# Optimization experiments

Hardware: AMD Instinct MI355X
Metric: run time of the kernel (lower is better)

The kernel has to match this reference:

```python
import jax, jax.numpy as jnp
import numpy as np

SIZES = [384, 160, 128, 96, 1]   # aev_length followed by hidden sizes (ANI-1 config)
N_SPECIES = 4                    # H, C, N, O
N_LAYERS = 4
CELU_ALPHA = 0.1
B, A = 128, 512                  # molecules, atoms per molecule


def setup_inputs() -> dict:
    key = jax.random.key(0)
    ks = jax.random.split(key, 2 + 2 * N_LAYERS)
    inp = {
        "fullaev": jax.random.normal(ks[0], (B, A, SIZES[0]), dtype=jnp.float32),
        "species": jax.random.randint(ks[1], (A,), 0, N_SPECIES, dtype=jnp.int32),
    }
    # Per-species stacked Linear params, torch default init: U(-1/sqrt(fan_in), 1/sqrt(fan_in))
    for l in range(N_LAYERS):
        bound = 1.0 / np.sqrt(SIZES[l])
        inp[f"W{l}"] = jax.random.uniform(ks[2 + 2 * l], (N_SPECIES, SIZES[l + 1], SIZES[l]),
                                          dtype=jnp.float32, minval=-bound, maxval=bound)
        inp[f"b{l}"] = jax.random.uniform(ks[3 + 2 * l], (N_SPECIES, SIZES[l + 1]),
                                          dtype=jnp.float32, minval=-bound, maxval=bound)
    return inp


def reference(fullaev, species, W0, b0, W1, b1, W2, b2, W3, b3):
    # fullaev: [B, A, aev_len]; species: [A] int route ids.
    # Equivalent to the per-atom Python loop: each atom goes through its
    # species' MLP; gather the per-atom weight matrices and do one batched GEMM per layer.
    Ws = (W0, W1, W2, W3)
    bs = (b0, b1, b2, b3)
    y = fullaev
    for l in range(N_LAYERS):
        Wa = Ws[l][species]          # [A, out, in] gathered per atom
        ba = bs[l][species]          # [A, out]
        y = jnp.einsum('bai,aoi->bao', y, Wa) + ba[None, :, :]
        if l < N_LAYERS - 1:
            y = jax.nn.celu(y, alpha=CELU_ALPHA)
    # stack over atoms + sum reducer over atom dim, then squeeze -> [B]
    return jnp.squeeze(jnp.sum(y, axis=1), axis=-1)
```

## Files before the change

kernel.cpp:

```cpp
#include <hip/hip_runtime.h>
#include <hip/hip_bf16.h>


typedef float f32x4 __attribute__((ext_vector_type(4)));
typedef short s16x8 __attribute__((ext_vector_type(8)));

#define NMOL   128
#define NATOM  512
#define AEV    384
#define MT     64
#define Y0LD   168
#define Y1LD   136
#define Y2LD   104
#define Y1_OFF 10752
#define RED_OFF 19456

#define PL0    61440
#define PL1    20480
#define PL2    12288
#define BASE0  0
#define BASE1  245760
#define BASE2  327680
#define WP_BYTE_OFF 262144

typedef const __attribute__((address_space(1))) void* gas_ptr;
typedef __attribute__((address_space(3))) void* las_ptr;

__device__ __forceinline__ ushort f2bf(float f) {
    uint u = __float_as_uint(f);
    return (ushort)((u + 0x7fffu + ((u >> 16) & 1u)) >> 16);
}
__device__ __forceinline__ float bf2f(ushort h) {
    return __uint_as_float(((uint)h) << 16);
}
__device__ __forceinline__ float celu_f(float v) {
    return fmaxf(v, 0.0f) + fminf(0.1f * (__expf(10.0f * v) - 1.0f), 0.0f);
}
__device__ __forceinline__ uint pk2bf(float x, float y) {
    __hip_bfloat162 h2;
    h2.x = __float2bfloat16(x);
    h2.y = __float2bfloat16(y);
    return *(uint*)&h2;
}

__global__ __launch_bounds__(256) void prep_kernel(
    const float* __restrict__ W0, const float* __restrict__ W1,
    const float* __restrict__ W2, ushort* __restrict__ Wp)
{
    const int idx = blockIdx.x * 256 + threadIdx.x;
    int n, k0, KS;
    size_t base;
    const float* src;
    if (idx < 30720) {
        const int s = idx / 7680, r = idx % 7680;
        n = r / 48; k0 = (r % 48) * 8; KS = 12;
        src = W0 + (size_t)idx * 8;
        base = BASE0 + (size_t)s * PL0;
    } else if (idx < 40960) {
        const int i2 = idx - 30720;
        const int s = i2 / 2560, r = i2 % 2560;
        n = r / 20; k0 = (r % 20) * 8; KS = 5;
        src = W1 + (size_t)i2 * 8;
        base = BASE1 + (size_t)s * PL1;
    } else {
        const int i2 = idx - 40960;
        const int s = i2 / 1536, r = i2 % 1536;
        n = r / 16; k0 = (r % 16) * 8; KS = 4;
        src = W2 + (size_t)i2 * 8;
        base = BASE2 + (size_t)s * PL2;
    }
    const float4 v0 = *(const float4*)(src);
    const float4 v1 = *(const float4*)(src + 4);
    const size_t fo = (size_t)((((n >> 4) * KS + (k0 >> 5)) * 64
                                + ((k0 & 31) >> 3) * 16 + (n & 15)) * 8);
    uint4 w;
    w.x = pk2bf(v0.x, v0.y);
    w.y = pk2bf(v0.z, v0.w);
    w.z = pk2bf(v1.x, v1.y);
    w.w = pk2bf(v1.z, v1.w);
    *(uint4*)(Wp + base + fo) = w;
}

__global__ __attribute__((amdgpu_flat_work_group_size(512, 512),
                          amdgpu_waves_per_eu(8, 8)))
void ani_mfma_kernel(
    const float* __restrict__ aev, const int* __restrict__ species,
    const ushort* __restrict__ Wp,
    const float* __restrict__ b0, const float* __restrict__ b1,
    const float* __restrict__ b2,
    const float* __restrict__ W3, const float* __restrict__ b3,
    float* __restrict__ partial)
{
    __shared__ __align__(16) ushort smem[20480];

    const int bid  = blockIdx.x;
    const int a    = bid >> 1;
    const int half = bid & 1;
    const int tid  = threadIdx.x;
    const int lane = tid & 63;
    const int wid  = tid >> 6;
    const int mgrp = wid >> 2;
    const int ngrp = wid & 3;
    const bool has3 = (ngrp < 2);

    const int s = species[a];
    const ushort* Bh0 = Wp + BASE0 + (size_t)s * PL0;
    const ushort* Bh1 = Wp + BASE1 + (size_t)s * PL1;
    const ushort* Bh2 = Wp + BASE2 + (size_t)s * PL2;
    const float* b0s = b0 + s * 160;
    const float* b1s = b1 + s * 128;
    const float* b2s = b2 + s * 96;
    const float* w3s = W3 + s * 96;
    const float  bb3 = b3[s];

    ushort* y0buf = smem;
    ushort* y1buf = smem + Y1_OFF;
    ushort* y2buf = smem;

    const int mol8 = lane >> 3;
    const int swz  = (lane & 7) ^ mol8;
    const char* gsrc = (const char*)(aev
        + ((size_t)(half * MT + wid * 8 + mol8) * NATOM + a) * AEV) + swz * 16;
    const int ldsbase = wid * 2048;

    const f32x4 zero = {0.f, 0.f, 0.f, 0.f};
    f32x4 acc[2][3];
    #pragma unroll
    for (int mf = 0; mf < 2; ++mf)
        #pragma unroll
        for (int ti = 0; ti < 3; ++ti) acc[mf][ti] = zero;

    {
        const int r0 = mgrp * 32 + (lane & 15);
        const int c2 = (lane >> 4) * 2;

        __builtin_amdgcn_global_load_lds((gas_ptr)(gsrc),
            (las_ptr)((char*)smem + ldsbase), 16, 0, 0);
        __builtin_amdgcn_global_load_lds((gas_ptr)(gsrc + 128),
            (las_ptr)((char*)smem + ldsbase + 1024), 16, 0, 0);
        __syncthreads();

        #pragma unroll
        for (int t = 0; t < 6; ++t) {
            if (t < 5) {
                const char* g = gsrc + (t + 1) * 256;
                char* d = (char*)smem + ((t + 1) & 1) * 16384 + ldsbase;
                __builtin_amdgcn_global_load_lds((gas_ptr)(g),       (las_ptr)(d),        16, 0, 0);
                __builtin_amdgcn_global_load_lds((gas_ptr)(g + 128), (las_ptr)(d + 1024), 16, 0, 0);
            }
            const float* Xb = (const float*)((const char*)smem + (t & 1) * 16384);
            #pragma unroll
            for (int gs = 0; gs < 2; ++gs) {
                const int gks = t * 2 + gs;
                const s16x8 bh0 = *(const s16x8*)(
                    Bh0 + ((size_t)((ngrp    ) * 12 + gks) * 64 + lane) * 8);
                const s16x8 bh1 = *(const s16x8*)(
                    Bh0 + ((size_t)((ngrp + 4) * 12 + gks) * 64 + lane) * 8);
                s16x8 bh2;
                if (has3) bh2 = *(const s16x8*)(
                    Bh0 + ((size_t)((ngrp + 8) * 12 + gks) * 64 + lane) * 8);

                s16x8 ah[2];
                #pragma unroll
                for (int mf = 0; mf < 2; ++mf) {
                    const int r = r0 + mf * 16;
                    const float* rp = Xb + (r >> 3) * 512 + gs * 256 + (r & 7) * 32;
                    const f32x4 v0 = *(const f32x4*)(rp + (((c2    ) ^ (r & 7)) * 4));
                    const f32x4 v1 = *(const f32x4*)(rp + (((c2 + 1) ^ (r & 7)) * 4));
                    union { s16x8 v; uint u[4]; } rr;
                    rr.u[0] = pk2bf(v0.x, v0.y);
                    rr.u[1] = pk2bf(v0.z, v0.w);
                    rr.u[2] = pk2bf(v1.x, v1.y);
                    rr.u[3] = pk2bf(v1.z, v1.w);
                    ah[mf] = rr.v;
                }
                acc[0][0] = __builtin_amdgcn_mfma_f32_16x16x32_bf16(ah[0], bh0, acc[0][0], 0, 0, 0);
                acc[1][0] = __builtin_amdgcn_mfma_f32_16x16x32_bf16(ah[1], bh0, acc[1][0], 0, 0, 0);
                acc[0][1] = __builtin_amdgcn_mfma_f32_16x16x32_bf16(ah[0], bh1, acc[0][1], 0, 0, 0);
                acc[1][1] = __builtin_amdgcn_mfma_f32_16x16x32_bf16(ah[1], bh1, acc[1][1], 0, 0, 0);
                if (has3) {
                    acc[0][2] = __builtin_amdgcn_mfma_f32_16x16x32_bf16(ah[0], bh2, acc[0][2], 0, 0, 0);
                    acc[1][2] = __builtin_amdgcn_mfma_f32_16x16x32_bf16(ah[1], bh2, acc[1][2], 0, 0, 0);
                }
            }
            __syncthreads();
        }
    }

    #pragma unroll
    for (int ti = 0; ti < 3; ++ti) {
        if (ti < 2 || has3) {
            const int n = (ngrp + 4 * ti) * 16 + (lane & 15);
            const float bv = b0s[n];
            #pragma unroll
            for (int mf = 0; mf < 2; ++mf) {
                #pragma unroll
                for (int r = 0; r < 4; ++r) {
                    const int row = mgrp * 32 + mf * 16 + (lane >> 4) * 4 + r;
                    y0buf[row * Y0LD + n] = f2bf(celu_f(acc[mf][ti][r] + bv));
                }
            }
        }
    }
    __syncthreads();

    f32x4 acc1[2][2];
    #pragma unroll
    for (int mf = 0; mf < 2; ++mf) { acc1[mf][0] = zero; acc1[mf][1] = zero; }
    {
        const ushort* arow0 = y0buf + (mgrp * 32 + (lane & 15)) * Y0LD + (lane >> 4) * 8;
        #pragma unroll
        for (int ks = 0; ks < 5; ++ks) {
            s16x8 ah[2];
            ah[0] = *(const s16x8*)(arow0 + ks * 32);
            ah[1] = *(const s16x8*)(arow0 + 16 * Y0LD + ks * 32);
            const s16x8 bh0 = *(const s16x8*)(
                Bh1 + ((size_t)((ngrp    ) * 5 + ks) * 64 + lane) * 8);
            const s16x8 bh1 = *(const s16x8*)(
                Bh1 + ((size_t)((ngrp + 4) * 5 + ks) * 64 + lane) * 8);
            acc1[0][0] = __builtin_amdgcn_mfma_f32_16x16x32_bf16(ah[0], bh0, acc1[0][0], 0, 0, 0);
            acc1[1][0] = __builtin_amdgcn_mfma_f32_16x16x32_bf16(ah[1], bh0, acc1[1][0], 0, 0, 0);
            acc1[0][1] = __builtin_amdgcn_mfma_f32_16x16x32_bf16(ah[0], bh1, acc1[0][1], 0, 0, 0);
            acc1[1][1] = __builtin_amdgcn_mfma_f32_16x16x32_bf16(ah[1], bh1, acc1[1][1], 0, 0, 0);
        }
    }

    #pragma unroll
    for (int t = 0; t < 2; ++t) {
        const int n = (ngrp + 4 * t) * 16 + (lane & 15);
        const float bv = b1s[n];
        #pragma unroll
        for (int mf = 0; mf < 2; ++mf) {
            #pragma unroll
            for (int r = 0; r < 4; ++r) {
                const int row = mgrp * 32 + mf * 16 + (lane >> 4) * 4 + r;
                y1buf[row * Y1LD + n] = f2bf(celu_f(acc1[mf][t][r] + bv));
            }
        }
    }
    __syncthreads();

    f32x4 acc2[2][2];
    #pragma unroll
    for (int mf = 0; mf < 2; ++mf) { acc2[mf][0] = zero; acc2[mf][1] = zero; }
    {
        const ushort* arow0 = y1buf + (mgrp * 32 + (lane & 15)) * Y1LD + (lane >> 4) * 8;
        #pragma unroll
        for (int ks = 0; ks < 4; ++ks) {
            s16x8 ah[2];
            ah[0] = *(const s16x8*)(arow0 + ks * 32);
            ah[1] = *(const s16x8*)(arow0 + 16 * Y1LD + ks * 32);
            const s16x8 bh0 = *(const s16x8*)(
                Bh2 + ((size_t)((ngrp) * 4 + ks) * 64 + lane) * 8);
            acc2[0][0] = __builtin_amdgcn_mfma_f32_16x16x32_bf16(ah[0], bh0, acc2[0][0], 0, 0, 0);
            acc2[1][0] = __builtin_amdgcn_mfma_f32_16x16x32_bf16(ah[1], bh0, acc2[1][0], 0, 0, 0);
            if (has3) {
                const s16x8 bh1 = *(const s16x8*)(
                    Bh2 + ((size_t)((ngrp + 4) * 4 + ks) * 64 + lane) * 8);
                acc2[0][1] = __builtin_amdgcn_mfma_f32_16x16x32_bf16(ah[0], bh1, acc2[0][1], 0, 0, 0);
                acc2[1][1] = __builtin_amdgcn_mfma_f32_16x16x32_bf16(ah[1], bh1, acc2[1][1], 0, 0, 0);
            }
        }
    }

    #pragma unroll
    for (int t = 0; t < 2; ++t) {
        if (t == 0 || has3) {
            const int n = (ngrp + 4 * t) * 16 + (lane & 15);
            const float bv = b2s[n];
            #pragma unroll
            for (int mf = 0; mf < 2; ++mf) {
                #pragma unroll
                for (int r = 0; r < 4; ++r) {
                    const int row = mgrp * 32 + mf * 16 + (lane >> 4) * 4 + r;
                    y2buf[row * Y2LD + n] = f2bf(celu_f(acc2[mf][t][r] + bv));
                }
            }
        }
    }
    __syncthreads();

    {
        float* red = (float*)(smem + RED_OFF);
        const int m = tid & (MT - 1);
        const int q = tid >> 6;
        float accv = 0.f;
        #pragma unroll
        for (int ii = 0; ii < 12; ++ii) {
            const int i = q * 12 + ii;
            accv = fmaf(w3s[i], bf2f(y2buf[m * Y2LD + i]), accv);
        }
        red[q * MT + m] = accv;
        __syncthreads();
        if (tid < MT) {
            float sm = bb3;
            #pragma unroll
            for (int qq = 0; qq < 8; ++qq) sm += red[qq * MT + tid];
            partial[(size_t)a * NMOL + half * MT + tid] = sm;
        }
    }
}

__global__ __launch_bounds__(256) void reduce_kernel(
    const float* __restrict__ partial, float* __restrict__ out)
{
    __shared__ float red[256];
    const int m = blockIdx.x;
    const int t = threadIdx.x;
    float sv = partial[(size_t)t * NMOL + m] + partial[(size_t)(t + 256) * NMOL + m];
    red[t] = sv;
    __syncthreads();
    #pragma unroll
    for (int w = 128; w > 0; w >>= 1) {
        if (t < w) red[t] += red[t + w];
        __syncthreads();
    }
    if (t == 0) out[m] = red[0];
}

extern "C" void kernel_launch(void* const* d_in, const int* in_sizes, int n_in,
                              void* d_out, int out_size, void* d_ws, size_t ws_size,
                              hipStream_t stream) {
    const float* aev     = (const float*)d_in[0];
    const int*   species = (const int*)  d_in[1];
    const float* W0 = (const float*)d_in[2];
    const float* b0 = (const float*)d_in[3];
    const float* W1 = (const float*)d_in[4];
    const float* b1 = (const float*)d_in[5];
    const float* W2 = (const float*)d_in[6];
    const float* b2 = (const float*)d_in[7];
    const float* W3 = (const float*)d_in[8];
    const float* b3 = (const float*)d_in[9];
    float* out     = (float*)d_out;
    float* partial = (float*)d_ws;
    ushort* Wp     = (ushort*)((char*)d_ws + WP_BYTE_OFF);

    prep_kernel<<<184, 256, 0, stream>>>(W0, W1, W2, Wp);
    ani_mfma_kernel<<<NATOM * 2, 512, 0, stream>>>(aev, species, Wp,
                                                   b0, b1, b2, W3, b3, partial);
    reduce_kernel<<<NMOL, 256, 0, stream>>>(partial, out);
}
```

Baseline: 44.12 us.

## Stage per-species weight fragments into LDS via async global-to-LDS loads

The bf16 weight fragments for all three MFMA layers are now copied into LDS with global_load_lds. Layer 0 is double-buffered alongside the AEV tiles, and layers 1 and 2 are staged while the previous epilogue runs. Before, every wave read the weights directly from global memory. The layer-0 packing in the prep kernel is reordered so each k-step slab is contiguous. LDS use grows from about 40KB to 72KB, the waves-per-EU target drops from 8 to 4, and the shared buffers get a new layout. The aim is to take weight-load latency off the MFMA path, at the cost of lower occupancy and an extra barrier.

```diff
diff --git a/kernel.cpp b/kernel.cpp
--- a/kernel.cpp
+++ b/kernel.cpp
@@ -12,8 +12,6 @@
 #define Y0LD   168
 #define Y1LD   136
 #define Y2LD   104
-#define Y1_OFF 10752
-#define RED_OFF 19456
 
 #define PL0    61440
 #define PL1    20480
@@ -48,31 +46,35 @@
     const float* __restrict__ W2, ushort* __restrict__ Wp)
 {
     const int idx = blockIdx.x * 256 + threadIdx.x;
-    int n, k0, KS;
-    size_t base;
+    size_t fo, base;
     const float* src;
     if (idx < 30720) {
         const int s = idx / 7680, r = idx % 7680;
-        n = r / 48; k0 = (r % 48) * 8; KS = 12;
+        const int n = r / 48, k0 = (r % 48) * 8;
+        const int t = k0 >> 6, h = (k0 >> 5) & 1;
+        fo = (size_t)t * 10240 + ((n >> 4) * 2 + h) * 512
+           + (((k0 & 31) >> 3) * 16 + (n & 15)) * 8;
         src = W0 + (size_t)idx * 8;
         base = BASE0 + (size_t)s * PL0;
     } else if (idx < 40960) {
         const int i2 = idx - 30720;
         const int s = i2 / 2560, r = i2 % 2560;
-        n = r / 20; k0 = (r % 20) * 8; KS = 5;
+        const int n = r / 20, k0 = (r % 20) * 8;
+        fo = (size_t)(((n >> 4) * 5 + (k0 >> 5)) * 64
+           + ((k0 & 31) >> 3) * 16 + (n & 15)) * 8;
         src = W1 + (size_t)i2 * 8;
         base = BASE1 + (size_t)s * PL1;
     } else {
         const int i2 = idx - 40960;
         const int s = i2 / 1536, r = i2 % 1536;
-        n = r / 16; k0 = (r % 16) * 8; KS = 4;
+        const int n = r / 16, k0 = (r % 16) * 8;
+        fo = (size_t)(((n >> 4) * 4 + (k0 >> 5)) * 64
+           + ((k0 & 31) >> 3) * 16 + (n & 15)) * 8;
         src = W2 + (size_t)i2 * 8;
         base = BASE2 + (size_t)s * PL2;
     }
     const float4 v0 = *(const float4*)(src);
     const float4 v1 = *(const float4*)(src + 4);
-    const size_t fo = (size_t)((((n >> 4) * KS + (k0 >> 5)) * 64
-                                + ((k0 & 31) >> 3) * 16 + (n & 15)) * 8);
     uint4 w;
     w.x = pk2bf(v0.x, v0.y);
     w.y = pk2bf(v0.z, v0.w);
@@ -82,7 +84,7 @@
 }
 
 __global__ __attribute__((amdgpu_flat_work_group_size(512, 512),
-                          amdgpu_waves_per_eu(8, 8)))
+                          amdgpu_waves_per_eu(4, 4)))
 void ani_mfma_kernel(
     const float* __restrict__ aev, const int* __restrict__ species,
     const ushort* __restrict__ Wp,
@@ -91,7 +93,8 @@
     const float* __restrict__ W3, const float* __restrict__ b3,
     float* __restrict__ partial)
 {
-    __shared__ __align__(16) ushort smem[20480];
+    __shared__ __align__(16) char smem8[73728];
+    ushort* smem_u = (ushort*)smem8;
 
     const int bid  = blockIdx.x;
     const int a    = bid >> 1;
@@ -113,9 +116,10 @@
     const float* w3s = W3 + s * 96;
     const float  bb3 = b3[s];
 
-    ushort* y0buf = smem;
-    ushort* y1buf = smem + Y1_OFF;
-    ushort* y2buf = smem;
+    ushort* y0buf = smem_u;
+    ushort* y1buf = smem_u;
+    ushort* y2buf = smem_u + 8704;
+    const ushort* BL = smem_u + 16384;
 
     const int mol8 = lane >> 3;
     const int swz  = (lane & 7) ^ mol8;
@@ -123,6 +127,19 @@
         + ((size_t)(half * MT + wid * 8 + mol8) * NATOM + a) * AEV) + swz * 16;
     const int ldsbase = wid * 2048;
 
+    auto stage_a = [&](int t, int b) {
+        const char* g = gsrc + t * 256;
+        char* d = smem8 + b * 16384 + ldsbase;
+        __builtin_amdgcn_global_load_lds((gas_ptr)(g),       (las_ptr)(d),        16, 0, 0);
+        __builtin_amdgcn_global_load_lds((gas_ptr)(g + 128), (las_ptr)(d + 1024), 16, 0, 0);
+    };
+    auto stage_b = [&](const ushort* gbase, int nchunks, int ldsbyte) {
+        for (int c = wid; c < nchunks; c += 8)
+            __builtin_amdgcn_global_load_lds(
+                (gas_ptr)((const char*)gbase + c * 1024 + lane * 16),
+                (las_ptr)(smem8 + ldsbyte + c * 1024), 16, 0, 0);
+    };
+
     const f32x4 zero = {0.f, 0.f, 0.f, 0.f};
     f32x4 acc[2][3];
     #pragma unroll
@@ -134,31 +151,25 @@
         const int r0 = mgrp * 32 + (lane & 15);
         const int c2 = (lane >> 4) * 2;
 
-        __builtin_amdgcn_global_load_lds((gas_ptr)(gsrc),
-            (las_ptr)((char*)smem + ldsbase), 16, 0, 0);
-        __builtin_amdgcn_global_load_lds((gas_ptr)(gsrc + 128),
-            (las_ptr)((char*)smem + ldsbase + 1024), 16, 0, 0);
+        stage_a(0, 0);
+        stage_b(Bh0, 20, 32768);
         __syncthreads();
 
         #pragma unroll
-        for (int t = 0; t < 6; ++t) {
-            if (t < 5) {
-                const char* g = gsrc + (t + 1) * 256;
-                char* d = (char*)smem + ((t + 1) & 1) * 16384 + ldsbase;
-                __builtin_amdgcn_global_load_lds((gas_ptr)(g),       (las_ptr)(d),        16, 0, 0);
-                __builtin_amdgcn_global_load_lds((gas_ptr)(g + 128), (las_ptr)(d + 1024), 16, 0, 0);
-            }
-            const float* Xb = (const float*)((const char*)smem + (t & 1) * 16384);
+        for (int tt = 0; tt < 6; ++tt) {
+            if (tt < 5) {
+                stage_a(tt + 1, (tt + 1) & 1);
+                stage_b(Bh0 + (size_t)(tt + 1) * 10240, 20,
+                        32768 + ((tt + 1) & 1) * 20480);
+            }
+            const float*  Xb = (const float*)(smem8 + (tt & 1) * 16384);
+            const ushort* Bl = BL + (tt & 1) * 10240;
             #pragma unroll
             for (int gs = 0; gs < 2; ++gs) {
-                const int gks = t * 2 + gs;
-                const s16x8 bh0 = *(const s16x8*)(
-                    Bh0 + ((size_t)((ngrp    ) * 12 + gks) * 64 + lane) * 8);
-                const s16x8 bh1 = *(const s16x8*)(
-                    Bh0 + ((size_t)((ngrp + 4) * 12 + gks) * 64 + lane) * 8);
+                const s16x8 bh0 = *(const s16x8*)(Bl + ((ngrp      * 2 + gs) * 512) + lane * 8);
+                const s16x8 bh1 = *(const s16x8*)(Bl + (((ngrp + 4) * 2 + gs) * 512) + lane * 8);
                 s16x8 bh2;
-                if (has3) bh2 = *(const s16x8*)(
-                    Bh0 + ((size_t)((ngrp + 8) * 12 + gks) * 64 + lane) * 8);
+                if (has3) bh2 = *(const s16x8*)(Bl + (((ngrp + 8) * 2 + gs) * 512) + lane * 8);
 
                 s16x8 ah[2];
                 #pragma unroll
@@ -187,6 +198,7 @@
         }
     }
 
+    stage_b(Bh1, 40, 32768);
     #pragma unroll
     for (int ti = 0; ti < 3; ++ti) {
         if (ti < 2 || has3) {
@@ -214,17 +226,17 @@
             s16x8 ah[2];
             ah[0] = *(const s16x8*)(arow0 + ks * 32);
             ah[1] = *(const s16x8*)(arow0 + 16 * Y0LD + ks * 32);
-            const s16x8 bh0 = *(const s16x8*)(
-                Bh1 + ((size_t)((ngrp    ) * 5 + ks) * 64 + lane) * 8);
-            const s16x8 bh1 = *(const s16x8*)(
-                Bh1 + ((size_t)((ngrp + 4) * 5 + ks) * 64 + lane) * 8);
+            const s16x8 bh0 = *(const s16x8*)(BL + ((ngrp      * 5 + ks) * 512) + lane * 8);
+            const s16x8 bh1 = *(const s16x8*)(BL + (((ngrp + 4) * 5 + ks) * 512) + lane * 8);
             acc1[0][0] = __builtin_amdgcn_mfma_f32_16x16x32_bf16(ah[0], bh0, acc1[0][0], 0, 0, 0);
             acc1[1][0] = __builtin_amdgcn_mfma_f32_16x16x32_bf16(ah[1], bh0, acc1[1][0], 0, 0, 0);
             acc1[0][1] = __builtin_amdgcn_mfma_f32_16x16x32_bf16(ah[0], bh1, acc1[0][1], 0, 0, 0);
             acc1[1][1] = __builtin_amdgcn_mfma_f32_16x16x32_bf16(ah[1], bh1, acc1[1][1], 0, 0, 0);
         }
     }
-
+    __syncthreads();
+
+    stage_b(Bh2, 24, 32768);
     #pragma unroll
     for (int t = 0; t < 2; ++t) {
         const int n = (ngrp + 4 * t) * 16 + (lane & 15);
@@ -250,13 +262,11 @@
             s16x8 ah[2];
             ah[0] = *(const s16x8*)(arow0 + ks * 32);
             ah[1] = *(const s16x8*)(arow0 + 16 * Y1LD + ks * 32);
-            const s16x8 bh0 = *(const s16x8*)(
-                Bh2 + ((size_t)((ngrp) * 4 + ks) * 64 + lane) * 8);
+            const s16x8 bh0 = *(const s16x8*)(BL + ((ngrp * 4 + ks) * 512) + lane * 8);
             acc2[0][0] = __builtin_amdgcn_mfma_f32_16x16x32_bf16(ah[0], bh0, acc2[0][0], 0, 0, 0);
             acc2[1][0] = __builtin_amdgcn_mfma_f32_16x16x32_bf16(ah[1], bh0, acc2[1][0], 0, 0, 0);
             if (has3) {
-                const s16x8 bh1 = *(const s16x8*)(
-                    Bh2 + ((size_t)((ngrp + 4) * 4 + ks) * 64 + lane) * 8);
+                const s16x8 bh1 = *(const s16x8*)(BL + (((ngrp + 4) * 4 + ks) * 512) + lane * 8);
                 acc2[0][1] = __builtin_amdgcn_mfma_f32_16x16x32_bf16(ah[0], bh1, acc2[0][1], 0, 0, 0);
                 acc2[1][1] = __builtin_amdgcn_mfma_f32_16x16x32_bf16(ah[1], bh1, acc2[1][1], 0, 0, 0);
             }
@@ -281,7 +291,7 @@
     __syncthreads();
 
     {
-        float* red = (float*)(smem + RED_OFF);
+        float* red = (float*)smem8;
         const int m = tid & (MT - 1);
         const int q = tid >> 6;
         float accv = 0.f;
```

New measurement: 44.30 us. No clear change (+0.4%).
